# Optimization experiments

Hardware: AMD Instinct MI355X
Metric: run time of the kernel (lower is better)

## Reference

```python
import jax, jax.numpy as jnp
import numpy as np

N_QUBITS = 8
DEPTH = 2
DIM = 2 ** N_QUBITS

# Hadamard gate (symmetric)
_H = (1.0 / np.sqrt(2.0)) * jnp.array([[1.0, 1.0], [1.0, -1.0]], dtype=jnp.complex64)
# sign table for <Z_i>: bit of wire i is bit (n-1-i) of the basis index (wire 0 = MSB)
_bits = (np.arange(DIM)[:, None] >> np.arange(N_QUBITS - 1, -1, -1)[None, :]) & 1
_SIGNS = jnp.asarray(1.0 - 2.0 * _bits, dtype=jnp.float32)  # [DIM, n_qubits]


def _quantum(ang):
    """Vectorized statevector simulation of the circuit:
    RX(ang_i) on each wire, then DEPTH x (CNOT ladder + H on last wire);
    returns <Z_i> for each wire. ang: [R, N_QUBITS] float32 -> [R, N_QUBITS]."""
    R = ang.shape[0]
    half = ang * 0.5
    a0 = jnp.cos(half).astype(jnp.complex64)
    a1 = (jnp.sin(half) * (-1j)).astype(jnp.complex64)  # RX|0> = cos|0> - i sin|1>
    single = jnp.stack([a0, a1], axis=-1)  # [R, n, 2]
    # product state via kron over qubits (wire 0 is the most significant factor)
    state = single[:, 0]  # [R, 2]
    for q in range(1, N_QUBITS):
        state = (state[:, :, None] * single[:, q][:, None, :]).reshape(R, -1)
    for _ in range(DEPTH):
        # CNOT ladder on adjacent wires (i -> i+1)
        for i in range(N_QUBITS - 1):
            s = state.reshape(R, 2 ** i, 2, 2, -1)  # [R, pre, ctrl, tgt, post]
            s = jnp.concatenate([s[:, :, :1], s[:, :, 1:, ::-1]], axis=2)
            state = s.reshape(R, -1)
        # Hadamard on the last wire
        s = state.reshape(R, -1, 2)
        state = (s @ _H).reshape(R, -1)
    probs = state.real ** 2 + state.imag ** 2  # [R, DIM]
    return probs @ _SIGNS  # [R, n_qubits]


def setup_inputs() -> dict:
    key = jax.random.key(0)
    k_x, k_w1, k_w2 = jax.random.split(key, 3)
    B, S, E, F = 8, 4096, 1024, N_QUBITS
    x = jax.random.normal(k_x, (B, S, E), dtype=jnp.float32)
    w1 = jax.random.normal(k_w1, (F, E), dtype=jnp.float32) * 0.02
    b1 = jnp.zeros((F,), dtype=jnp.float32)
    w2 = jax.random.normal(k_w2, (E, F), dtype=jnp.float32) * 0.02
    b2 = jnp.zeros((E,), dtype=jnp.float32)
    return {"x": x, "w1": w1, "b1": b1, "w2": w2, "b2": b2}


def reference(x, w1, b1, w2, b2):
    B, S, E = x.shape
    h = jnp.einsum('bse,fe->bsf', x, w1) + b1  # linear1 -> [B, S, ffn_dim]
    q = _quantum(h.reshape(-1, N_QUBITS)).reshape(B, S, N_QUBITS)
    # dropout is identity in eval mode
    return jnp.einsum('bsf,ef->bse', q, w2) + b2  # linear2 -> [B, S, E]
```

## Files before the change

### kernel.cpp

```cpp
#include <hip/hip_runtime.h>


typedef float f4 __attribute__((ext_vector_type(4)));

constexpr int THREADS = 256;
constexpr int TILE    = 8;
constexpr int E       = 1024;
constexpr int R_TOTAL = 8 * 4096;

template<int CTRL>
__device__ __forceinline__ float dppf(float v) {
    return __int_as_float(__builtin_amdgcn_update_dpp(
        0, __float_as_int(v), CTRL, 0xF, 0xF, true));
}

__global__ __launch_bounds__(THREADS, 4)
void ffq_kernel(const float* __restrict__ x,
                const float* __restrict__ w1,
                const float* __restrict__ b1,
                const float* __restrict__ w2,
                const float* __restrict__ b2,
                float* __restrict__ out)
{
    __shared__ __align__(16) float lds_x[TILE * E];
    __shared__ float part[TILE * 16 * 9];
    __shared__ __align__(16) float qsh[TILE][8];
    __shared__ float b1s[8];

    const int t    = threadIdx.x;
    const int lane = t & 63;
    const int wid  = t >> 6;
    const int c0   = t * 4;

    const int row0 = blockIdx.x * TILE;

#pragma unroll
    for (int r = 0; r < TILE; ++r) {
        __builtin_amdgcn_global_load_lds(
            (const __attribute__((address_space(1))) void*)
                (x + (size_t)(row0 + r) * E + wid * 256 + lane * 4),
            (__attribute__((address_space(3))) void*)
                (&lds_x[r * E + wid * 256]),
            16, 0, 0);
    }

    if (t < 8) b1s[t] = b1[t];
    f4 w1r[8];
#pragma unroll
    for (int f = 0; f < 8; ++f)
        w1r[f] = *(const f4*)(w1 + f * E + c0);

    const bool writer = (lane & 12) == 0;
    const int  jj     = wid * 4 + (lane >> 4);
    const int  fb     = lane & 3;

    asm volatile("s_waitcnt vmcnt(0)" ::: "memory");

#pragma unroll
    for (int s = 0; s < TILE; ++s) {
        const f4 xc = *(const f4*)(&lds_x[s * E + t * 4]);

        float h[8];
#pragma unroll
        for (int f = 0; f < 8; ++f)
            h[f] = xc.x * w1r[f].x + xc.y * w1r[f].y
                 + xc.z * w1r[f].z + xc.w * w1r[f].w;

        {
            const bool hb = lane & 1;
            float s0 = hb ? h[0] : h[1];
            float s1 = hb ? h[2] : h[3];
            float s2 = hb ? h[4] : h[5];
            float s3 = hb ? h[6] : h[7];
            s0 = dppf<0xB1>(s0); s1 = dppf<0xB1>(s1);
            s2 = dppf<0xB1>(s2); s3 = dppf<0xB1>(s3);
            h[0] = (hb ? h[1] : h[0]) + s0;
            h[1] = (hb ? h[3] : h[2]) + s1;
            h[2] = (hb ? h[5] : h[4]) + s2;
            h[3] = (hb ? h[7] : h[6]) + s3;
        }
        float v0, v1;
        {
            const bool hb = lane & 2;
            float s0 = hb ? h[0] : h[1];
            float s1 = hb ? h[2] : h[3];
            s0 = dppf<0x4E>(s0); s1 = dppf<0x4E>(s1);
            v0 = (hb ? h[1] : h[0]) + s0;
            v1 = (hb ? h[3] : h[2]) + s1;
        }
        v0 += dppf<0x124>(v0);  v1 += dppf<0x124>(v1);
        v0 += dppf<0x128>(v0);  v1 += dppf<0x128>(v1);

        if (writer) {
            const int w = (s * 16 + jj) * 9 + fb;
            part[w]     = v0;
            part[w + 4] = v1;
        }
    }
    __syncthreads();

    if (t < TILE * 8) {
        const int r = t >> 3;
        const int f = t & 7;
        float hq = b1s[f];
#pragma unroll
        for (int j = 0; j < 16; ++j)
            hq += part[(r * 16 + j) * 9 + f];
        float p = __cosf(hq);
        float u = __shfl_up(p, 2, 8); if (f >= 2) p *= u;
        u = __shfl_up(p, 4, 8);       if (f >= 4) p *= u;
        const float p6 = __shfl(p, 6, 8);
        if (f == 7) p *= p6;
        qsh[r][f] = p;
    }

    float w2a[4][8];
#pragma unroll
    for (int j = 0; j < 4; ++j) {
        const f4 lo = *(const f4*)(w2 + (size_t)(c0 + j) * 8);
        const f4 hi = *(const f4*)(w2 + (size_t)(c0 + j) * 8 + 4);
        w2a[j][0] = lo.x; w2a[j][1] = lo.y; w2a[j][2] = lo.z; w2a[j][3] = lo.w;
        w2a[j][4] = hi.x; w2a[j][5] = hi.y; w2a[j][6] = hi.z; w2a[j][7] = hi.w;
    }
    const f4 b2v = *(const f4*)(b2 + c0);

    __syncthreads();

#pragma unroll
    for (int s = 0; s < TILE; ++s) {
        const f4 qlo = *(const f4*)(&qsh[s][0]);
        const f4 qhi = *(const f4*)(&qsh[s][4]);
        const float qv[8] = {qlo.x, qlo.y, qlo.z, qlo.w,
                             qhi.x, qhi.y, qhi.z, qhi.w};
        f4 o = b2v;
#pragma unroll
        for (int f = 0; f < 8; ++f) {
            o.x += qv[f] * w2a[0][f];
            o.y += qv[f] * w2a[1][f];
            o.z += qv[f] * w2a[2][f];
            o.w += qv[f] * w2a[3][f];
        }
        __builtin_nontemporal_store(o, (f4*)(out + (size_t)(row0 + s) * E + c0));
    }
}

extern "C" void kernel_launch(void* const* d_in, const int* in_sizes, int n_in,
                              void* d_out, int out_size, void* d_ws, size_t ws_size,
                              hipStream_t stream)
{
    const float* x  = (const float*)d_in[0];
    const float* w1 = (const float*)d_in[1];
    const float* b1 = (const float*)d_in[2];
    const float* w2 = (const float*)d_in[3];
    const float* b2 = (const float*)d_in[4];
    float* out = (float*)d_out;

    ffq_kernel<<<dim3(R_TOTAL / TILE), THREADS, 0, stream>>>(x, w1, b1, w2, b2, out);
}
```

Baseline: 241.1 us.

## Double-buffer x row chunks in LDS and process more rows per block

Each block now handles 16 rows instead of 8, split into four 4-row chunks. The chunks are staged into two LDS buffers with global_load_lds, so the load of the next chunk overlaps the linear1 dot products on the current one. This targets exposed global-load latency and per-block setup cost, since w1 and w2 register loads are amortized over more rows. In exchange the grid has half as many blocks. The waitcnt(4) count assumes exactly four outstanding loads per chunk, and the only barrier comes after all chunks, so LDS visibility across waves relies on each wave reading only the rows it staged itself.

```diff
diff --git a/kernel.cpp b/kernel.cpp
--- a/kernel.cpp
+++ b/kernel.cpp
@@ -4,7 +4,9 @@
 typedef float f4 __attribute__((ext_vector_type(4)));
 
 constexpr int THREADS = 256;
-constexpr int TILE    = 8;
+constexpr int CR      = 4;
+constexpr int NC      = 4;
+constexpr int BR      = CR * NC;
 constexpr int E       = 1024;
 constexpr int R_TOTAL = 8 * 4096;
 
@@ -12,6 +14,22 @@
 __device__ __forceinline__ float dppf(float v) {
     return __int_as_float(__builtin_amdgcn_update_dpp(
         0, __float_as_int(v), CTRL, 0xF, 0xF, true));
+}
+
+__device__ __forceinline__ void stage_chunk(const float* __restrict__ x,
+                                            float* lds_buf,
+                                            int row0, int chunk,
+                                            int wid, int lane)
+{
+#pragma unroll
+    for (int r = 0; r < CR; ++r) {
+        __builtin_amdgcn_global_load_lds(
+            (const __attribute__((address_space(1))) void*)
+                (x + (size_t)(row0 + chunk * CR + r) * E + wid * 256 + lane * 4),
+            (__attribute__((address_space(3))) void*)
+                (lds_buf + r * E + wid * 256),
+            16, 0, 0);
+    }
 }
 
 __global__ __launch_bounds__(THREADS, 4)
@@ -22,9 +40,9 @@
                 const float* __restrict__ b2,
                 float* __restrict__ out)
 {
-    __shared__ __align__(16) float lds_x[TILE * E];
-    __shared__ float part[TILE * 16 * 9];
-    __shared__ __align__(16) float qsh[TILE][8];
+    __shared__ __align__(16) float lds_x[2][CR * E];
+    __shared__ float part[BR * 16 * 9];
+    __shared__ __align__(16) float qsh[BR][8];
     __shared__ float b1s[8];
 
     const int t    = threadIdx.x;
@@ -32,17 +50,7 @@
     const int wid  = t >> 6;
     const int c0   = t * 4;
 
-    const int row0 = blockIdx.x * TILE;
-
-#pragma unroll
-    for (int r = 0; r < TILE; ++r) {
-        __builtin_amdgcn_global_load_lds(
-            (const __attribute__((address_space(1))) void*)
-                (x + (size_t)(row0 + r) * E + wid * 256 + lane * 4),
-            (__attribute__((address_space(3))) void*)
-                (&lds_x[r * E + wid * 256]),
-            16, 0, 0);
-    }
+    const int row0 = blockIdx.x * BR;
 
     if (t < 8) b1s[t] = b1[t];
     f4 w1r[8];
@@ -54,52 +62,65 @@
     const int  jj     = wid * 4 + (lane >> 4);
     const int  fb     = lane & 3;
 
-    asm volatile("s_waitcnt vmcnt(0)" ::: "memory");
+    stage_chunk(x, &lds_x[0][0], row0, 0, wid, lane);
 
 #pragma unroll
-    for (int s = 0; s < TILE; ++s) {
-        const f4 xc = *(const f4*)(&lds_x[s * E + t * 4]);
+    for (int c = 0; c < NC; ++c) {
+        const int buf = c & 1;
 
-        float h[8];
+        if (c + 1 < NC) {
+            stage_chunk(x, &lds_x[buf ^ 1][0], row0, c + 1, wid, lane);
+            asm volatile("s_waitcnt vmcnt(4)" ::: "memory");
+        } else {
+            asm volatile("s_waitcnt vmcnt(0)" ::: "memory");
+        }
+
 #pragma unroll
-        for (int f = 0; f < 8; ++f)
-            h[f] = xc.x * w1r[f].x + xc.y * w1r[f].y
-                 + xc.z * w1r[f].z + xc.w * w1r[f].w;
+        for (int s = 0; s < CR; ++s) {
+            const int rb = c * CR + s;
+            const f4 xc = *(const f4*)(&lds_x[buf][s * E + t * 4]);
 
-        {
-            const bool hb = lane & 1;
-            float s0 = hb ? h[0] : h[1];
-            float s1 = hb ? h[2] : h[3];
-            float s2 = hb ? h[4] : h[5];
-            float s3 = hb ? h[6] : h[7];
-            s0 = dppf<0xB1>(s0); s1 = dppf<0xB1>(s1);
-            s2 = dppf<0xB1>(s2); s3 = dppf<0xB1>(s3);
-            h[0] = (hb ? h[1] : h[0]) + s0;
-            h[1] = (hb ? h[3] : h[2]) + s1;
-            h[2] = (hb ? h[5] : h[4]) + s2;
-            h[3] = (hb ? h[7] : h[6]) + s3;
-        }
-        float v0, v1;
-        {
-            const bool hb = lane & 2;
-            float s0 = hb ? h[0] : h[1];
-            float s1 = hb ? h[2] : h[3];
-            s0 = dppf<0x4E>(s0); s1 = dppf<0x4E>(s1);
-            v0 = (hb ? h[1] : h[0]) + s0;
-            v1 = (hb ? h[3] : h[2]) + s1;
-        }
-        v0 += dppf<0x124>(v0);  v1 += dppf<0x124>(v1);
-        v0 += dppf<0x128>(v0);  v1 += dppf<0x128>(v1);
+            float h[8];
+#pragma unroll
+            for (int f = 0; f < 8; ++f)
+                h[f] = xc.x * w1r[f].x + xc.y * w1r[f].y
+                     + xc.z * w1r[f].z + xc.w * w1r[f].w;
 
-        if (writer) {
-            const int w = (s * 16 + jj) * 9 + fb;
-            part[w]     = v0;
-            part[w + 4] = v1;
+            {
+                const bool hb = lane & 1;
+                float s0 = hb ? h[0] : h[1];
+                float s1 = hb ? h[2] : h[3];
+                float s2 = hb ? h[4] : h[5];
+                float s3 = hb ? h[6] : h[7];
+                s0 = dppf<0xB1>(s0); s1 = dppf<0xB1>(s1);
+                s2 = dppf<0xB1>(s2); s3 = dppf<0xB1>(s3);
+                h[0] = (hb ? h[1] : h[0]) + s0;
+                h[1] = (hb ? h[3] : h[2]) + s1;
+                h[2] = (hb ? h[5] : h[4]) + s2;
+                h[3] = (hb ? h[7] : h[6]) + s3;
+            }
+            float v0, v1;
+            {
+                const bool hb = lane & 2;
+                float s0 = hb ? h[0] : h[1];
+                float s1 = hb ? h[2] : h[3];
+                s0 = dppf<0x4E>(s0); s1 = dppf<0x4E>(s1);
+                v0 = (hb ? h[1] : h[0]) + s0;
+                v1 = (hb ? h[3] : h[2]) + s1;
+            }
+            v0 += dppf<0x124>(v0);  v1 += dppf<0x124>(v1);
+            v0 += dppf<0x128>(v0);  v1 += dppf<0x128>(v1);
+
+            if (writer) {
+                const int w = (rb * 16 + jj) * 9 + fb;
+                part[w]     = v0;
+                part[w + 4] = v1;
+            }
         }
     }
     __syncthreads();
 
-    if (t < TILE * 8) {
+    if (t < BR * 8) {
         const int r = t >> 3;
         const int f = t & 7;
         float hq = b1s[f];
@@ -127,7 +148,7 @@
     __syncthreads();
 
 #pragma unroll
-    for (int s = 0; s < TILE; ++s) {
+    for (int s = 0; s < BR; ++s) {
         const f4 qlo = *(const f4*)(&qsh[s][0]);
         const f4 qhi = *(const f4*)(&qsh[s][4]);
         const float qv[8] = {qlo.x, qlo.y, qlo.z, qlo.w,
@@ -155,5 +176,5 @@
     const float* b2 = (const float*)d_in[4];
     float* out = (float*)d_out;
 
-    ffq_kernel<<<dim3(R_TOTAL / TILE), THREADS, 0, stream>>>(x, w1, b1, w2, b2, out);
+    ffq_kernel<<<dim3(R_TOTAL / BR), THREADS, 0, stream>>>(x, w1, b1, w2, b2, out);
 }
```

Measured after the change: 243.5 us. No clear change (+1.0%).
